# Optimization experiments

Hardware: AMD Instinct MI355X
Metric: run time of the kernel (lower is better)

The kernel has to match this reference:

```python
import jax, jax.numpy as jnp
import numpy as np

N_NODES = 100000
N_EDGES = 1600000
D_IN = 128
D_OUT = 128


def setup_inputs() -> dict:
    key = jax.random.key(0)
    k1, k2, k3, k4, k5 = jax.random.split(key, 5)
    features = jax.random.normal(k1, (N_NODES, D_IN), dtype=jnp.float32)
    weight = jax.random.normal(k2, (D_IN, D_OUT), dtype=jnp.float32)
    edge_val = jax.random.uniform(k3, (N_EDGES,), dtype=jnp.float32)
    edge_row = jax.random.randint(k4, (N_EDGES,), 0, N_NODES, dtype=jnp.int32)
    edge_col = jax.random.randint(k5, (N_EDGES,), 0, N_NODES, dtype=jnp.int32)
    return {"features": features, "weight": weight, "edge_val": edge_val,
            "edge_row": edge_row, "edge_col": edge_col}


def reference(features, weight, edge_val, edge_row, edge_col):
    # support = features @ W   (dense GEMM; torch.spmm with dense-strided lhs)
    support = features @ weight  # [N, D_OUT]
    # output = pre @ support   (sparse COO adjacency spmm)
    msgs = edge_val[:, None] * support[edge_col]  # [E, D_OUT] gather
    output = jax.ops.segment_sum(msgs, edge_row, num_segments=N_NODES)  # scatter-add
    # act == 'relu'; dropout p=0.0 is identity
    return jax.nn.relu(output)
```

## Files before the change

kernel.cpp:

```cpp
#include <hip/hip_runtime.h>
#include <hip/hip_bf16.h>


#define N_NODES 100000
#define N_EDGES 1600000
#define D 128
#define GEMM_BLOCKS ((N_NODES + 63) / 64)
#define CHUNK_A 8192
#define NBLK_A ((N_EDGES + CHUNK_A - 1) / CHUNK_A)
#define BUCKETS ((N_NODES + 127) / 128)
#define N_SCAN (BUCKETS * NBLK_A)
#define SCAN_BLK ((N_SCAN + 1023) / 1024)
#define BCAP 4608

typedef __attribute__((ext_vector_type(8))) short short8;
typedef __attribute__((ext_vector_type(4))) float floatx4;
typedef int  iv2 __attribute__((ext_vector_type(2)));
typedef int  iv4 __attribute__((ext_vector_type(4)));
typedef float fv4 __attribute__((ext_vector_type(4)));

union U16B { uint4 u4; short8 s8; uint u[4]; ushort us[8]; };

__device__ __forceinline__ ushort f32_to_bf16(float f) {
    uint b = __float_as_uint(f);
    return (ushort)((b + 0x7FFFu + ((b >> 16) & 1u)) >> 16);
}
__device__ __forceinline__ float bf16_to_f32(ushort u) {
    return __uint_as_float((uint)u << 16);
}

__global__ __launch_bounds__(256) void wconv_kernel(const float* __restrict__ W,
                                                    ushort* __restrict__ WB,
                                                    uint* __restrict__ st) {
    const int o = blockIdx.x * 256 + threadIdx.x;
    if (o < D * D) {
        const int K8 = o >> 10, rem = o & 1023, n = rem >> 3, j = rem & 7;
        WB[o] = f32_to_bf16(W[(K8 * 8 + j) * D + n]);
    }
    if (st && blockIdx.x == 0 && threadIdx.x < 256) st[threadIdx.x] = 0u;
}

__global__ __launch_bounds__(256) void gemm_kernel(const float* __restrict__ feat,
                                                   const ushort* __restrict__ WB,
                                                   ushort* __restrict__ support,
                                                   const int* __restrict__ edge_row,
                                                   int* __restrict__ histT) {
    const int bid = blockIdx.x, tid = threadIdx.x;
    if (histT != nullptr && bid < NBLK_A) {
        __shared__ int hist[BUCKETS];
        for (int i = tid; i < BUCKETS; i += 256) hist[i] = 0;
        __syncthreads();
        const int base = bid * CHUNK_A;
        #pragma unroll
        for (int k = 0; k < CHUNK_A / 256; k++) {
            const int e = base + k * 256 + tid;
            if (e < N_EDGES) atomicAdd(&hist[edge_row[e] >> 7], 1);
        }
        __syncthreads();
        for (int i = tid; i < BUCKETS; i += 256) histT[i * NBLK_A + bid] = hist[i];
        return;
    }
    const int gbid = (histT != nullptr) ? bid - NBLK_A : bid;

    const int wave = tid >> 6, lane = tid & 63;
    const int row0 = gbid * 64 + wave * 16;
    const int m = lane & 15, g = lane >> 4;
    if (row0 >= N_NODES) return;

    floatx4 acc[8];
    const floatx4 z = {0.f, 0.f, 0.f, 0.f};
    #pragma unroll
    for (int t = 0; t < 8; t++) acc[t] = z;

    const float* arow = feat + (size_t)(row0 + m) * D;
    const ushort* wb = WB + g * 1024 + m * 8;
    #pragma unroll
    for (int s = 0; s < 4; s++) {
        float4 a0 = *(const float4*)(arow + s * 32 + g * 8);
        float4 a1 = *(const float4*)(arow + s * 32 + g * 8 + 4);
        U16B a;
        a.us[0] = f32_to_bf16(a0.x); a.us[1] = f32_to_bf16(a0.y);
        a.us[2] = f32_to_bf16(a0.z); a.us[3] = f32_to_bf16(a0.w);
        a.us[4] = f32_to_bf16(a1.x); a.us[5] = f32_to_bf16(a1.y);
        a.us[6] = f32_to_bf16(a1.z); a.us[7] = f32_to_bf16(a1.w);
        #pragma unroll
        for (int t = 0; t < 8; t++) {
            U16B b; b.u4 = *(const uint4*)(wb + s * 4096 + t * 128);
            acc[t] = __builtin_amdgcn_mfma_f32_16x16x32_bf16(b.s8, a.s8, acc[t], 0, 0, 0);
        }
    }
    ushort* srow = support + (size_t)(row0 + m) * D + g * 4;
    #pragma unroll
    for (int t = 0; t < 8; t++) {
        union { ushort us[4]; uint2 u2; } o;
        #pragma unroll
        for (int r = 0; r < 4; r++) o.us[r] = f32_to_bf16(acc[t][r]);
        *(uint2*)(srow + t * 16) = o.u2;
    }
}

__global__ __launch_bounds__(1024) void scan_kernel(const int* __restrict__ histT,
                                                    int* __restrict__ baseST,
                                                    int* __restrict__ bucketOff,
                                                    uint* __restrict__ st) {
    __shared__ int wsum[16];
    __shared__ int s_run, s_base;
    const int tid = threadIdx.x, b = blockIdx.x;
    const int gid = b * 1024 + tid;
    const int lane = tid & 63, wave = tid >> 6;

    const int v = (gid < N_SCAN) ? histT[gid] : 0;
    int x = v;
    #pragma unroll
    for (int d = 1; d < 64; d <<= 1) {
        int y = __shfl_up(x, d, 64);
        if (lane >= d) x += y;
    }
    if (lane == 63) wsum[wave] = x;
    __syncthreads();
    if (tid == 0) {
        int run = 0;
        #pragma unroll
        for (int w = 0; w < 16; w++) { int t = wsum[w]; wsum[w] = run; run += t; }
        s_run = run;
        __hip_atomic_store(&st[b], (1u << 30) | (uint)run,
                           __ATOMIC_RELEASE, __HIP_MEMORY_SCOPE_AGENT);
    }
    __syncthreads();
    if (wave == 0) {
        int P = 0;
        int base = b;
        bool done = (b == 0);
        while (!done) {
            const int j = base - 1 - lane;
            uint w;
            if (j >= 0) {
                do {
                    w = __hip_atomic_load(&st[j], __ATOMIC_ACQUIRE, __HIP_MEMORY_SCOPE_AGENT);
                } while ((w >> 30) == 0u);
            } else w = 2u << 30;
            const unsigned long long m2 = __ballot((w >> 30) == 2u);
            int contrib;
            if (m2) {
                const int fl = (int)__ffsll(m2) - 1;
                contrib = (lane <= fl) ? (int)(w & 0x3FFFFFFFu) : 0;
                done = true;
            } else {
                contrib = (int)(w & 0x3FFFFFFFu);
                base -= 64;
            }
            #pragma unroll
            for (int mm = 1; mm < 64; mm <<= 1) contrib += __shfl_xor(contrib, mm, 64);
            P += contrib;
        }
        if (lane == 0) {
            __hip_atomic_store(&st[b], (2u << 30) | (uint)(P + s_run),
                               __ATOMIC_RELEASE, __HIP_MEMORY_SCOPE_AGENT);
            s_base = P;
        }
    }
    __syncthreads();
    if (gid < N_SCAN) {
        const int excl = s_base + wsum[wave] + (x - v);
        const int bucket = gid / NBLK_A;
        const int blk = gid - bucket * NBLK_A;
        baseST[blk * BUCKETS + bucket] = excl;
        if (blk == 0) bucketOff[bucket] = excl;
    }
    if (gid == 0) bucketOff[BUCKETS] = N_EDGES;
}

__global__ __launch_bounds__(1024) void binscatter_kernel(const int* __restrict__ edge_row,
                                                          const int* __restrict__ edge_col,
                                                          const float* __restrict__ edge_val,
                                                          const int* __restrict__ baseST,
                                                          iv2* __restrict__ sorted) {
    __shared__ int cur[BUCKETS];
    const int tid = threadIdx.x, blk = blockIdx.x;
    for (int i = tid; i < BUCKETS; i += 1024) cur[i] = baseST[blk * BUCKETS + i];
    __syncthreads();
    const int base = blk * CHUNK_A;
    #pragma unroll
    for (int k = 0; k < CHUNK_A / 1024; k += 2) {
        const int e0 = base + k * 1024 + tid;
        const int e1 = e0 + 1024;
        const bool v0 = (e0 < N_EDGES), v1 = (e1 < N_EDGES);
        int r0 = 0, c0 = 0, r1 = 0, c1 = 0;
        float w0 = 0.f, w1 = 0.f;
        if (v0) { r0 = edge_row[e0]; c0 = edge_col[e0]; w0 = edge_val[e0]; }
        if (v1) { r1 = edge_row[e1]; c1 = edge_col[e1]; w1 = edge_val[e1]; }
        if (v0) {
            const int p = atomicAdd(&cur[r0 >> 7], 1);
            iv2 pk; pk.x = ((r0 & 127) << 17) | c0; pk.y = __float_as_int(w0);
            sorted[p] = pk;
        }
        if (v1) {
            const int p = atomicAdd(&cur[r1 >> 7], 1);
            iv2 pk; pk.x = ((r1 & 127) << 17) | c1; pk.y = __float_as_int(w1);
            sorted[p] = pk;
        }
    }
}

__global__ __launch_bounds__(1024) void bucket_accum_kernel(const int* __restrict__ bucketOff,
                                                            const iv2* __restrict__ sorted,
                                                            const ushort* __restrict__ support,
                                                            float* __restrict__ out) {
    __shared__ iv2 sldsE[BCAP];
    __shared__ int cnt[128], rowStart[128], cur[128];
    __shared__ int wtot;
    const int tid = threadIdx.x, b = blockIdx.x;
    const int s = bucketOff[b];
    const int nE = bucketOff[b + 1] - s;

    if (tid < 128) cnt[tid] = 0;
    __syncthreads();

    iv2 h0, h1, h2, h3, h4;
    {
        int i = tid;
        if (i < nE) { h0 = sorted[s + i]; i += 1024; }
        if (i < nE) { h1 = sorted[s + i]; i += 1024; }
        if (i < nE) { h2 = sorted[s + i]; i += 1024; }
        if (i < nE) { h3 = sorted[s + i]; i += 1024; }
        if (i < nE) { h4 = sorted[s + i]; }
    }
    {
        int i = tid;
        if (i < nE) { atomicAdd(&cnt[h0.x >> 17], 1); i += 1024; }
        if (i < nE) { atomicAdd(&cnt[h1.x >> 17], 1); i += 1024; }
        if (i < nE) { atomicAdd(&cnt[h2.x >> 17], 1); i += 1024; }
        if (i < nE) { atomicAdd(&cnt[h3.x >> 17], 1); i += 1024; }
        if (i < nE) { atomicAdd(&cnt[h4.x >> 17], 1); }
    }
    __syncthreads();
    const int lane = tid & 63;
    const int myc = (tid < 128) ? cnt[tid] : 0;
    int x = myc;
    #pragma unroll
    for (int d = 1; d < 64; d <<= 1) {
        int y = __shfl_up(x, d, 64);
        if (lane >= d) x += y;
    }
    if (tid == 63) wtot = x;
    __syncthreads();
    if (tid < 128) {
        const int excl = x - myc + ((tid >= 64) ? wtot : 0);
        rowStart[tid] = excl;
        cur[tid] = excl;
    }
    __syncthreads();
    {
        int i = tid;
        if (i < nE) { sldsE[atomicAdd(&cur[h0.x >> 17], 1)] = h0; i += 1024; }
        if (i < nE) { sldsE[atomicAdd(&cur[h1.x >> 17], 1)] = h1; i += 1024; }
        if (i < nE) { sldsE[atomicAdd(&cur[h2.x >> 17], 1)] = h2; i += 1024; }
        if (i < nE) { sldsE[atomicAdd(&cur[h3.x >> 17], 1)] = h3; i += 1024; }
        if (i < nE) { sldsE[atomicAdd(&cur[h4.x >> 17], 1)] = h4; }
    }
    __syncthreads();

    const int g = tid >> 4, part = tid & 15;
    #pragma unroll
    for (int t = 0; t < 2; t++) {
        const int rl = g * 2 + t;
        const int grow = (b << 7) + rl;
        if (grow >= N_NODES) break;
        const int rs = rowStart[rl], re = rs + cnt[rl];

        float acc0[8], acc1[8];
        #pragma unroll
        for (int i = 0; i < 8; i++) { acc0[i] = 0.f; acc1[i] = 0.f; }

        int k = rs;
        for (; k + 3 < re; k += 4) {
            const iv2 e0 = sldsE[k], e1 = sldsE[k + 1];
            const iv2 e2 = sldsE[k + 2], e3 = sldsE[k + 3];
            U16B s0; s0.u4 = *(const uint4*)(support + (size_t)(e0.x & 0x1FFFF) * D + part * 8);
            U16B s1; s1.u4 = *(const uint4*)(support + (size_t)(e1.x & 0x1FFFF) * D + part * 8);
            U16B s2; s2.u4 = *(const uint4*)(support + (size_t)(e2.x & 0x1FFFF) * D + part * 8);
            U16B s3; s3.u4 = *(const uint4*)(support + (size_t)(e3.x & 0x1FFFF) * D + part * 8);
            const float v0 = __int_as_float(e0.y);
            const float v1 = __int_as_float(e1.y);
            const float v2 = __int_as_float(e2.y);
            const float v3 = __int_as_float(e3.y);
            #pragma unroll
            for (int i = 0; i < 8; i++) {
                acc0[i] += bf16_to_f32(s0.us[i]) * v0;
                acc1[i] += bf16_to_f32(s1.us[i]) * v1;
                acc0[i] += bf16_to_f32(s2.us[i]) * v2;
                acc1[i] += bf16_to_f32(s3.us[i]) * v3;
            }
        }
        for (; k < re; ++k) {
            const iv2 e0 = sldsE[k];
            U16B s0; s0.u4 = *(const uint4*)(support + (size_t)(e0.x & 0x1FFFF) * D + part * 8);
            const float v0 = __int_as_float(e0.y);
            #pragma unroll
            for (int i = 0; i < 8; i++) acc0[i] += bf16_to_f32(s0.us[i]) * v0;
        }

        fv4 lo, hi;
        lo.x = fmaxf(acc0[0] + acc1[0], 0.f); lo.y = fmaxf(acc0[1] + acc1[1], 0.f);
        lo.z = fmaxf(acc0[2] + acc1[2], 0.f); lo.w = fmaxf(acc0[3] + acc1[3], 0.f);
        hi.x = fmaxf(acc0[4] + acc1[4], 0.f); hi.y = fmaxf(acc0[5] + acc1[5], 0.f);
        hi.z = fmaxf(acc0[6] + acc1[6], 0.f); hi.w = fmaxf(acc0[7] + acc1[7], 0.f);
        float* dst = out + (size_t)grow * D + part * 8;
        __builtin_nontemporal_store(lo, (fv4*)dst);
        __builtin_nontemporal_store(hi, (fv4*)(dst + 4));
    }
}

__global__ __launch_bounds__(256) void zero_f4_kernel(float4* __restrict__ acc, int n4) {
    int i = blockIdx.x * 256 + threadIdx.x;
    if (i < n4) acc[i] = make_float4(0.f, 0.f, 0.f, 0.f);
}
__global__ __launch_bounds__(256) void spmm_kernel(const ushort* __restrict__ support,
                                                   const float* __restrict__ edge_val,
                                                   const int* __restrict__ edge_row,
                                                   const int* __restrict__ edge_col,
                                                   float* __restrict__ out) {
    const long gtid = (long)blockIdx.x * 256 + threadIdx.x;
    const int edge = (int)(gtid >> 4);
    const int part = (int)(gtid & 15);
    if (edge >= N_EDGES) return;
    const int col = edge_col[edge];
    const int row = edge_row[edge];
    const float v = edge_val[edge];
    U16B s; s.u4 = *(const uint4*)(support + (size_t)col * D + part * 8);
    float* dst = out + (size_t)row * D + part * 8;
    #pragma unroll
    for (int i = 0; i < 8; i++) unsafeAtomicAdd(dst + i, bf16_to_f32(s.us[i]) * v);
}
__global__ __launch_bounds__(256) void relu_kernel(float4* __restrict__ out, int n4) {
    int i = blockIdx.x * 256 + threadIdx.x;
    if (i >= n4) return;
    float4 a = out[i];
    a.x = fmaxf(a.x, 0.f); a.y = fmaxf(a.y, 0.f);
    a.z = fmaxf(a.z, 0.f); a.w = fmaxf(a.w, 0.f);
    out[i] = a;
}

extern "C" void kernel_launch(void* const* d_in, const int* in_sizes, int n_in,
                              void* d_out, int out_size, void* d_ws, size_t ws_size,
                              hipStream_t stream) {
    (void)in_sizes; (void)n_in; (void)out_size;
    const float* feat     = (const float*)d_in[0];
    const float* W        = (const float*)d_in[1];
    const float* edge_val = (const float*)d_in[2];
    const int*   edge_row = (const int*)d_in[3];
    const int*   edge_col = (const int*)d_in[4];
    float* out = (float*)d_out;

    char* ws = (char*)d_ws;
    size_t o = 0;
    ushort* support  = (ushort*)(ws + o); o += (size_t)N_NODES * D * sizeof(ushort);
    ushort* WB       = (ushort*)(ws + o); o += (size_t)D * D * sizeof(ushort);
    int*    histT    = (int*)(ws + o);    o += ((size_t)N_SCAN * 4 + 15) & ~15ull;
    int*    baseST   = (int*)(ws + o);    o += ((size_t)N_SCAN * 4 + 15) & ~15ull;
    int*    bucketOff= (int*)(ws + o);    o += ((size_t)(BUCKETS + 1) * 4 + 15) & ~15ull;
    uint*   st       = (uint*)(ws + o);   o += 256 * 4;
    iv2*    sorted   = (iv2*)(ws + o);    o += (size_t)N_EDGES * 8;
    const size_t needed = o;

    if (ws_size >= needed) {
        wconv_kernel<<<(D * D + 255) / 256, 256, 0, stream>>>(W, WB, st);
        gemm_kernel<<<NBLK_A + GEMM_BLOCKS, 256, 0, stream>>>(feat, WB, support, edge_row,
                                                              histT);
        scan_kernel<<<SCAN_BLK, 1024, 0, stream>>>(histT, baseST, bucketOff, st);
        binscatter_kernel<<<NBLK_A, 1024, 0, stream>>>(edge_row, edge_col, edge_val,
                                                       baseST, sorted);
        bucket_accum_kernel<<<BUCKETS, 1024, 0, stream>>>(bucketOff, sorted, support, out);
    } else {
        const int n4 = N_NODES * D / 4;
        zero_f4_kernel<<<(n4 + 255) / 256, 256, 0, stream>>>((float4*)out, n4);
        wconv_kernel<<<(D * D + 255) / 256, 256, 0, stream>>>(W, WB, nullptr);
        gemm_kernel<<<GEMM_BLOCKS, 256, 0, stream>>>(feat, WB, support, nullptr, nullptr);
        spmm_kernel<<<(int)(((long)N_EDGES * 16 + 255) / 256), 256, 0, stream>>>(
            support, edge_val, edge_row, edge_col, out);
        relu_kernel<<<(n4 + 255) / 256, 256, 0, stream>>>((float4*)out, n4);
    }
}
```

Measured before the change: 229.9 us.

## Merge weight conversion with histogram and co-schedule GEMM with bin scatter

Weight conversion to bf16 is folded into the edge-histogram launch, so it no longer needs its own kernel. The dense GEMM is moved out of that launch and fused with the bin-scatter kernel, with blocks split by index, so the GEMM runs concurrently with the scatter. This cuts one kernel launch and lets compute-bound MFMA work overlap the memory-bound scatter. In exchange, the GEMM now runs in 1024-thread blocks covering 256 rows each, which changes occupancy. The scatter blocks also share LDS allocation with the GEMM blocks.

```diff
diff --git a/kernel.cpp b/kernel.cpp
--- a/kernel.cpp
+++ b/kernel.cpp
@@ -5,7 +5,8 @@
 #define N_NODES 100000
 #define N_EDGES 1600000
 #define D 128
-#define GEMM_BLOCKS ((N_NODES + 63) / 64)
+#define WCONV_BLOCKS ((D * D + 255) / 256)
+#define GEMM_BLOCKS_K2 ((N_NODES + 255) / 256)
 #define CHUNK_A 8192
 #define NBLK_A ((N_EDGES + CHUNK_A - 1) / CHUNK_A)
 #define BUCKETS ((N_NODES + 127) / 128)
@@ -29,74 +30,33 @@
     return __uint_as_float((uint)u << 16);
 }
 
-__global__ __launch_bounds__(256) void wconv_kernel(const float* __restrict__ W,
-                                                    ushort* __restrict__ WB,
-                                                    uint* __restrict__ st) {
-    const int o = blockIdx.x * 256 + threadIdx.x;
-    if (o < D * D) {
-        const int K8 = o >> 10, rem = o & 1023, n = rem >> 3, j = rem & 7;
-        WB[o] = f32_to_bf16(W[(K8 * 8 + j) * D + n]);
-    }
-    if (st && blockIdx.x == 0 && threadIdx.x < 256) st[threadIdx.x] = 0u;
-}
-
-__global__ __launch_bounds__(256) void gemm_kernel(const float* __restrict__ feat,
-                                                   const ushort* __restrict__ WB,
-                                                   ushort* __restrict__ support,
+__global__ __launch_bounds__(256) void prep_kernel(const float* __restrict__ W,
+                                                   ushort* __restrict__ WB,
+                                                   uint* __restrict__ st,
                                                    const int* __restrict__ edge_row,
                                                    int* __restrict__ histT) {
     const int bid = blockIdx.x, tid = threadIdx.x;
-    if (histT != nullptr && bid < NBLK_A) {
-        __shared__ int hist[BUCKETS];
-        for (int i = tid; i < BUCKETS; i += 256) hist[i] = 0;
-        __syncthreads();
-        const int base = bid * CHUNK_A;
-        #pragma unroll
-        for (int k = 0; k < CHUNK_A / 256; k++) {
-            const int e = base + k * 256 + tid;
-            if (e < N_EDGES) atomicAdd(&hist[edge_row[e] >> 7], 1);
-        }
-        __syncthreads();
-        for (int i = tid; i < BUCKETS; i += 256) histT[i * NBLK_A + bid] = hist[i];
+    if (bid < WCONV_BLOCKS || histT == nullptr) {
+        const int o = bid * 256 + tid;
+        if (o < D * D) {
+            const int K8 = o >> 10, rem = o & 1023, n = rem >> 3, j = rem & 7;
+            WB[o] = f32_to_bf16(W[(K8 * 8 + j) * D + n]);
+        }
+        if (st && bid == 0 && tid < 256) st[tid] = 0u;
         return;
     }
-    const int gbid = (histT != nullptr) ? bid - NBLK_A : bid;
-
-    const int wave = tid >> 6, lane = tid & 63;
-    const int row0 = gbid * 64 + wave * 16;
-    const int m = lane & 15, g = lane >> 4;
-    if (row0 >= N_NODES) return;
-
-    floatx4 acc[8];
-    const floatx4 z = {0.f, 0.f, 0.f, 0.f};
-    #pragma unroll
-    for (int t = 0; t < 8; t++) acc[t] = z;
-
-    const float* arow = feat + (size_t)(row0 + m) * D;
-    const ushort* wb = WB + g * 1024 + m * 8;
-    #pragma unroll
-    for (int s = 0; s < 4; s++) {
-        float4 a0 = *(const float4*)(arow + s * 32 + g * 8);
-        float4 a1 = *(const float4*)(arow + s * 32 + g * 8 + 4);
-        U16B a;
-        a.us[0] = f32_to_bf16(a0.x); a.us[1] = f32_to_bf16(a0.y);
-        a.us[2] = f32_to_bf16(a0.z); a.us[3] = f32_to_bf16(a0.w);
-        a.us[4] = f32_to_bf16(a1.x); a.us[5] = f32_to_bf16(a1.y);
-        a.us[6] = f32_to_bf16(a1.z); a.us[7] = f32_to_bf16(a1.w);
-        #pragma unroll
-        for (int t = 0; t < 8; t++) {
-            U16B b; b.u4 = *(const uint4*)(wb + s * 4096 + t * 128);
-            acc[t] = __builtin_amdgcn_mfma_f32_16x16x32_bf16(b.s8, a.s8, acc[t], 0, 0, 0);
-        }
-    }
-    ushort* srow = support + (size_t)(row0 + m) * D + g * 4;
-    #pragma unroll
-    for (int t = 0; t < 8; t++) {
-        union { ushort us[4]; uint2 u2; } o;
-        #pragma unroll
-        for (int r = 0; r < 4; r++) o.us[r] = f32_to_bf16(acc[t][r]);
-        *(uint2*)(srow + t * 16) = o.u2;
-    }
+    __shared__ int hist[BUCKETS];
+    const int hbid = bid - WCONV_BLOCKS;
+    for (int i = tid; i < BUCKETS; i += 256) hist[i] = 0;
+    __syncthreads();
+    const int base = hbid * CHUNK_A;
+    #pragma unroll
+    for (int k = 0; k < CHUNK_A / 256; k++) {
+        const int e = base + k * 256 + tid;
+        if (e < N_EDGES) atomicAdd(&hist[edge_row[e] >> 7], 1);
+    }
+    __syncthreads();
+    for (int i = tid; i < BUCKETS; i += 256) histT[i * NBLK_A + hbid] = hist[i];
 }
 
 __global__ __launch_bounds__(1024) void scan_kernel(const int* __restrict__ histT,
@@ -170,35 +130,79 @@
     if (gid == 0) bucketOff[BUCKETS] = N_EDGES;
 }
 
-__global__ __launch_bounds__(1024) void binscatter_kernel(const int* __restrict__ edge_row,
-                                                          const int* __restrict__ edge_col,
-                                                          const float* __restrict__ edge_val,
-                                                          const int* __restrict__ baseST,
-                                                          iv2* __restrict__ sorted) {
+__global__ __launch_bounds__(1024) void fused_kernel(const float* __restrict__ feat,
+                                                     const ushort* __restrict__ WB,
+                                                     ushort* __restrict__ support,
+                                                     const int* __restrict__ edge_row,
+                                                     const int* __restrict__ edge_col,
+                                                     const float* __restrict__ edge_val,
+                                                     const int* __restrict__ baseST,
+                                                     iv2* __restrict__ sorted,
+                                                     int nScatter) {
     __shared__ int cur[BUCKETS];
-    const int tid = threadIdx.x, blk = blockIdx.x;
-    for (int i = tid; i < BUCKETS; i += 1024) cur[i] = baseST[blk * BUCKETS + i];
-    __syncthreads();
-    const int base = blk * CHUNK_A;
-    #pragma unroll
-    for (int k = 0; k < CHUNK_A / 1024; k += 2) {
-        const int e0 = base + k * 1024 + tid;
-        const int e1 = e0 + 1024;
-        const bool v0 = (e0 < N_EDGES), v1 = (e1 < N_EDGES);
-        int r0 = 0, c0 = 0, r1 = 0, c1 = 0;
-        float w0 = 0.f, w1 = 0.f;
-        if (v0) { r0 = edge_row[e0]; c0 = edge_col[e0]; w0 = edge_val[e0]; }
-        if (v1) { r1 = edge_row[e1]; c1 = edge_col[e1]; w1 = edge_val[e1]; }
-        if (v0) {
-            const int p = atomicAdd(&cur[r0 >> 7], 1);
-            iv2 pk; pk.x = ((r0 & 127) << 17) | c0; pk.y = __float_as_int(w0);
-            sorted[p] = pk;
-        }
-        if (v1) {
-            const int p = atomicAdd(&cur[r1 >> 7], 1);
-            iv2 pk; pk.x = ((r1 & 127) << 17) | c1; pk.y = __float_as_int(w1);
-            sorted[p] = pk;
-        }
+    const int bid = blockIdx.x, tid = threadIdx.x;
+    if (bid < nScatter) {
+        const int blk = bid;
+        for (int i = tid; i < BUCKETS; i += 1024) cur[i] = baseST[blk * BUCKETS + i];
+        __syncthreads();
+        const int base = blk * CHUNK_A;
+        #pragma unroll
+        for (int k = 0; k < CHUNK_A / 1024; k += 2) {
+            const int e0 = base + k * 1024 + tid;
+            const int e1 = e0 + 1024;
+            const bool v0 = (e0 < N_EDGES), v1 = (e1 < N_EDGES);
+            int r0 = 0, c0 = 0, r1 = 0, c1 = 0;
+            float w0 = 0.f, w1 = 0.f;
+            if (v0) { r0 = edge_row[e0]; c0 = edge_col[e0]; w0 = edge_val[e0]; }
+            if (v1) { r1 = edge_row[e1]; c1 = edge_col[e1]; w1 = edge_val[e1]; }
+            if (v0) {
+                const int p = atomicAdd(&cur[r0 >> 7], 1);
+                iv2 pk; pk.x = ((r0 & 127) << 17) | c0; pk.y = __float_as_int(w0);
+                sorted[p] = pk;
+            }
+            if (v1) {
+                const int p = atomicAdd(&cur[r1 >> 7], 1);
+                iv2 pk; pk.x = ((r1 & 127) << 17) | c1; pk.y = __float_as_int(w1);
+                sorted[p] = pk;
+            }
+        }
+        return;
+    }
+    const int gbid = bid - nScatter;
+    const int wave = tid >> 6, lane = tid & 63;
+    const int row0 = gbid * 256 + wave * 16;
+    const int m = lane & 15, g = lane >> 4;
+    if (row0 >= N_NODES) return;
+
+    floatx4 acc[8];
+    const floatx4 z = {0.f, 0.f, 0.f, 0.f};
+    #pragma unroll
+    for (int t = 0; t < 8; t++) acc[t] = z;
+
+    const float* arow = feat + (size_t)(row0 + m) * D;
+    const ushort* wb = WB + g * 1024 + m * 8;
+    #pragma unroll
+    for (int s = 0; s < 4; s++) {
+        float4 a0 = *(const float4*)(arow + s * 32 + g * 8);
+        float4 a1 = *(const float4*)(arow + s * 32 + g * 8 + 4);
+        U16B a;
+        a.us[0] = f32_to_bf16(a0.x); a.us[1] = f32_to_bf16(a0.y);
+        a.us[2] = f32_to_bf16(a0.z); a.us[3] = f32_to_bf16(a0.w);
+        a.us[4] = f32_to_bf16(a1.x); a.us[5] = f32_to_bf16(a1.y);
+        a.us[6] = f32_to_bf16(a1.z); a.us[7] = f32_to_bf16(a1.w);
+        #pragma unroll
+        for (int t = 0; t < 8; t++) {
+            U16B b; b.u4 = *(const uint4*)(wb + s * 4096 + t * 128);
+            acc[t] = __builtin_amdgcn_mfma_f32_16x16x32_bf16(b.s8, a.s8, acc[t], 0, 0, 0);
+        }
+    }
+    ushort* srow = support + (size_t)(row0 + m) * D + g * 4;
+    #pragma unroll
+    for (int t = 0; t < 8; t++) {
+        union { ushort us[4]; uint2 u2; } o;
+        #pragma unroll
+        for (int r = 0; r < 4; r++) o.us[r] = f32_to_bf16(acc[t][r]);
+        *(uint2*)(srow + t * 16) = o.u2;
     }
 }
 
@@ -364,18 +368,17 @@
     const size_t needed = o;
 
     if (ws_size >= needed) {
-        wconv_kernel<<<(D * D + 255) / 256, 256, 0, stream>>>(W, WB, st);
-        gemm_kernel<<<NBLK_A + GEMM_BLOCKS, 256, 0, stream>>>(feat, WB, support, edge_row,
-                                                              histT);
+        prep_kernel<<<WCONV_BLOCKS + NBLK_A, 256, 0, stream>>>(W, WB, st, edge_row, histT);
         scan_kernel<<<SCAN_BLK, 1024, 0, stream>>>(histT, baseST, bucketOff, st);
-        binscatter_kernel<<<NBLK_A, 1024, 0, stream>>>(edge_row, edge_col, edge_val,
-                                                       baseST, sorted);
+        fused_kernel<<<NBLK_A + GEMM_BLOCKS_K2, 1024, 0, stream>>>(
+            feat, WB, support, edge_row, edge_col, edge_val, baseST, sorted, NBLK_A);
         bucket_accum_kernel<<<BUCKETS, 1024, 0, stream>>>(bucketOff, sorted, support, out);
     } else {
         const int n4 = N_NODES * D / 4;
         zero_f4_kernel<<<(n4 + 255) / 256, 256, 0, stream>>>((float4*)out, n4);
-        wconv_kernel<<<(D * D + 255) / 256, 256, 0, stream>>>(W, WB, nullptr);
-        gemm_kernel<<<GEMM_BLOCKS, 256, 0, stream>>>(feat, WB, support, nullptr, nullptr);
+        prep_kernel<<<WCONV_BLOCKS, 256, 0, stream>>>(W, WB, nullptr, nullptr, nullptr);
+        fused_kernel<<<GEMM_BLOCKS_K2, 1024, 0, stream>>>(
+            feat, WB, support, nullptr, nullptr, nullptr, nullptr, nullptr, 0);
         spmm_kernel<<<(int)(((long)N_EDGES * 16 + 255) / 256), 256, 0, stream>>>(
             support, edge_val, edge_row, edge_col, out);
         relu_kernel<<<(n4 + 255) / 256, 256, 0, stream>>>((float4*)out, n4);
```

Measured after the change: 247.1 us. +7.5%, slower.
